# Performance work log

Hardware: AMD Instinct MI355X
Metric: run time of the kernel (lower is better)

The kernel has to match this reference:

```python
import jax, jax.numpy as jnp
import numpy as np
import math

B, N, E, H = 2, 10000, 160000, 128
ET = 8
EPS = 1e-5


def setup_inputs() -> dict:
    key = jax.random.key(0)
    ks = jax.random.split(key, 20)
    s = 1.0 / math.sqrt(H)
    inp = {
        "hidden": jax.random.normal(ks[0], (B, N, H), jnp.float32),
        "time_emb": jax.random.normal(ks[1], (B, N, H), jnp.float32),
        "edge_index": jax.random.randint(ks[2], (2, E), 0, N),
        "edge_type": jax.random.randint(ks[3], (E,), 0, ET),
        # parameters
        "edge_emb": jax.random.normal(ks[4], (ET, H), jnp.float32),
        "Wq": jax.random.normal(ks[5], (H, H), jnp.float32) * s,
        "bq": jnp.zeros((H,), jnp.float32),
        "Wk": jax.random.normal(ks[6], (H, H), jnp.float32) * s,
        "bk": jnp.zeros((H,), jnp.float32),
        "Wv": jax.random.normal(ks[7], (H, H), jnp.float32) * s,
        "bv": jnp.zeros((H,), jnp.float32),
        "We": jax.random.normal(ks[8], (H, 1), jnp.float32) * s,
        "be": jnp.zeros((1,), jnp.float32),
        "W1": jax.random.normal(ks[9], (3 * H, H), jnp.float32) * (1.0 / math.sqrt(3 * H)),
        "b1": jnp.zeros((H,), jnp.float32),
        "W2": jax.random.normal(ks[10], (H, H), jnp.float32) * s,
        "b2": jnp.zeros((H,), jnp.float32),
        "gamma": jnp.ones((H,), jnp.float32),
        "beta": jnp.zeros((H,), jnp.float32),
    }
    return inp


def _forward(hidden, time_emb, edge_index, edge_type, edge_emb,
             Wq, bq, Wk, bk, Wv, bv, We, be, W1, b1, W2, b2, gamma, beta):
    src, tgt = edge_index[0], edge_index[1]
    # edge-wise gathers: [B, E, H]
    src_h = hidden[:, src]
    tgt_h = hidden[:, tgt]
    src_t = time_emb[:, src]
    tgt_t = time_emb[:, tgt]
    edge_h = edge_emb[edge_type][None, :, :]  # [1, E, H] broadcasts over batch

    query = (tgt_h + tgt_t) @ Wq + bq
    key = (src_h + src_t + edge_h) @ Wk + bk
    value = (src_h + edge_h) @ Wv + bv

    logits = jnp.einsum("beh,beh->be", query, key) / math.sqrt(H)
    logits = logits + (edge_h @ We + be)[..., 0]  # edge bias broadcast over batch

    # segment softmax per target node (equivalent to the per-node masked softmax loop)
    lT = logits.T  # [E, B]
    seg_max = jax.ops.segment_max(lT, tgt, num_segments=N)          # [N, B]
    seg_max = jnp.where(jnp.isfinite(seg_max), seg_max, 0.0)
    ex = jnp.exp(lT - seg_max[tgt])                                  # [E, B]
    seg_sum = jax.ops.segment_sum(ex, tgt, num_segments=N)           # [N, B]
    weights = (ex / seg_sum[tgt]).T                                  # [B, E]

    messages = value * weights[..., None]                            # [B, E, H]
    # scatter-add to target nodes
    agg = jax.ops.segment_sum(jnp.swapaxes(messages, 0, 1), tgt, num_segments=N)  # [N, B, H]
    aggregated = jnp.swapaxes(agg, 0, 1)                             # [B, N, H]

    cat = jnp.concatenate([hidden, aggregated, time_emb], axis=-1)   # [B, N, 3H]
    updated = jax.nn.silu(cat @ W1 + b1) @ W2 + b2

    x = hidden + updated  # dropout p=0 -> identity
    mu = jnp.mean(x, axis=-1, keepdims=True)
    var = jnp.var(x, axis=-1, keepdims=True)
    return (x - mu) * jax.lax.rsqrt(var + EPS) * gamma + beta


def reference(hidden, time_emb, edge_index, edge_type, edge_emb,
              Wq, bq, Wk, bk, Wv, bv, We, be, W1, b1, W2, b2, gamma, beta):
    return _forward(hidden, time_emb, edge_index, edge_type, edge_emb,
                    Wq, bq, Wk, bk, Wv, bv, We, be, W1, b1, W2, b2, gamma, beta)
```

## Files before the change

kernel.cpp:

```cpp
#include <hip/hip_runtime.h>
#include <math.h>

constexpr int B_  = 2;
constexpr int N_  = 10000;
constexpr int E_  = 160000;
constexpr int H_  = 128;
constexpr int ET_ = 8;
constexpr float EPS_ = 1e-5f;
constexpr float RSQH = 0.08838834764831845f;

typedef __bf16 bf16x8 __attribute__((ext_vector_type(8)));
typedef short  short8 __attribute__((ext_vector_type(8)));
typedef float  f32x4  __attribute__((ext_vector_type(4)));
typedef unsigned short u16;

__device__ inline u16 bf16b(float f) {
    return __builtin_bit_cast(u16, (__bf16)f);
}

__device__ inline bf16x8 ldfrag(const u16* __restrict__ W, int kc, int nt, int lane) {
    short8 s = *(const short8*)(W + ((kc * 8 + nt) * 64 + lane) * 8);
    return __builtin_bit_cast(bf16x8, s);
}

__global__ __launch_bounds__(256)
void setup_kernel(const float* __restrict__ W1, const float* __restrict__ W2,
                  const float* __restrict__ Wq, const float* __restrict__ Wk,
                  const float* __restrict__ Wv,
                  u16* __restrict__ W1s, u16* __restrict__ W2s,
                  u16* __restrict__ Wqs, u16* __restrict__ Wks, u16* __restrict__ Wvs,
                  const float* __restrict__ edge_emb,
                  const float* __restrict__ bk, const float* __restrict__ bv,
                  const float* __restrict__ We, const float* __restrict__ be,
                  float* __restrict__ Kt, float* __restrict__ Vt, float* __restrict__ eb,
                  const int* __restrict__ tgt, int* __restrict__ hist)
{
    const int bid = blockIdx.x, tid = threadIdx.x;
    if (bid < 56) {
        int unit = bid >> 1, half = bid & 1;
        const float* src; u16* dst; int kc;
        if (unit < 12)      { src = W1; dst = W1s; kc = unit; }
        else if (unit < 16) { src = W2; dst = W2s; kc = unit - 12; }
        else if (unit < 20) { src = Wq; dst = Wqs; kc = unit - 16; }
        else if (unit < 24) { src = Wk; dst = Wks; kc = unit - 20; }
        else                { src = Wv; dst = Wvs; kc = unit - 24; }
        int nt = half * 4 + (tid >> 6), lane = tid & 63;
        int q = lane >> 4, c = lane & 15;
        int kbase = kc * 32 + q * 8;
        int col = nt * 16 + c;
        u16* out = dst + ((kc * 8 + nt) * 64 + lane) * 8;
#pragma unroll
        for (int j = 0; j < 8; ++j)
            out[j] = bf16b(src[(kbase + j) * H_ + col]);
    } else if (bid < 64) {
        int t = bid - 56;
        const float* ep = edge_emb + t * H_;
        __shared__ float red[2];
        int j = tid;
        if (j < 128) {
            float ak = bk[j], av = bv[j];
            for (int d = 0; d < H_; d += 4) {
                float e0 = ep[d], e1 = ep[d+1], e2 = ep[d+2], e3 = ep[d+3];
                ak += e0*Wk[(d+0)*H_+j] + e1*Wk[(d+1)*H_+j] + e2*Wk[(d+2)*H_+j] + e3*Wk[(d+3)*H_+j];
                av += e0*Wv[(d+0)*H_+j] + e1*Wv[(d+1)*H_+j] + e2*Wv[(d+2)*H_+j] + e3*Wv[(d+3)*H_+j];
            }
            Kt[t*H_ + j] = ak;
            Vt[t*H_ + j] = av;
            float pe = ep[j] * We[j];
#pragma unroll
            for (int off = 32; off; off >>= 1) pe += __shfl_xor(pe, off);
            if ((j & 63) == 0) red[j >> 6] = pe;
        }
        __syncthreads();
        if (j == 0) eb[t] = red[0] + red[1] + be[0];
    } else {
        int e = (bid - 64) * 256 + tid;
        if (e < E_) atomicAdd(&hist[tgt[e]], 1);
    }
}

__global__ __launch_bounds__(1024)
void scan_kernel(const int* __restrict__ hist, int* __restrict__ offs,
                 int* __restrict__ cursor)
{
    __shared__ int winc[16];
    const int tid = threadIdx.x, wave = tid >> 6, lane = tid & 63;
    int v[10];
    const int idx0 = tid * 10;
    int tot = 0;
#pragma unroll
    for (int i = 0; i < 10; ++i) {
        int idx = idx0 + i;
        v[i] = (idx < N_) ? hist[idx] : 0;
        tot += v[i];
    }
    int s = tot;
#pragma unroll
    for (int off = 1; off < 64; off <<= 1) {
        int t = __shfl_up(s, off);
        if (lane >= off) s += t;
    }
    if (lane == 63) winc[wave] = s;
    __syncthreads();
    if (tid < 16) {
        int si = winc[tid];
#pragma unroll
        for (int off = 1; off < 16; off <<= 1) {
            int t = __shfl_up(si, off);
            if (tid >= off) si += t;
        }
        winc[tid] = si;
    }
    __syncthreads();
    int wbase = (wave == 0) ? 0 : winc[wave - 1];
    int run = wbase + (s - tot);
#pragma unroll
    for (int i = 0; i < 10; ++i) {
        int idx = idx0 + i;
        if (idx < N_) { offs[idx] = run; cursor[idx] = run; }
        run += v[i];
    }
    if (tid == 0) offs[N_] = winc[15];
}

__global__ __launch_bounds__(256)
void scatter_qkv_kernel(const int* __restrict__ src, const int* __restrict__ tgt,
                        const int* __restrict__ type, int* __restrict__ cursor,
                        int* __restrict__ sorted,
                        const float* __restrict__ hidden, const float* __restrict__ time_emb,
                        const u16* __restrict__ Wqs, const u16* __restrict__ Wks,
                        const u16* __restrict__ Wvs, const float* __restrict__ bq,
                        u16* __restrict__ Q, u16* __restrict__ K, u16* __restrict__ V)
{
    if (blockIdx.x < 625) {
        int e = blockIdx.x * 256 + threadIdx.x;
        if (e < E_) {
            int t = tgt[e];
            int pos = atomicAdd(&cursor[t], 1);
            sorted[pos] = src[e] | (type[e] << 16);
        }
        return;
    }
    const int wv = threadIdx.x >> 6, lane = threadIdx.x & 63;
    const int tile = (blockIdx.x - 625) * 4 + wv;
    if (tile >= (B_ * N_) / 16) return;
    const int nbase = tile * 16;
    const int m = lane & 15, q = lane >> 4;
    const int koff = q * 8;

    bf16x8 aq[4], av[4];
    const float* hp = hidden   + (nbase + m) * H_ + koff;
    const float* tp = time_emb + (nbase + m) * H_ + koff;
#pragma unroll
    for (int kc = 0; kc < 4; ++kc) {
        float4 h0 = *(const float4*)(hp + kc * 32);
        float4 h1 = *(const float4*)(hp + kc * 32 + 4);
        float4 t0 = *(const float4*)(tp + kc * 32);
        float4 t1 = *(const float4*)(tp + kc * 32 + 4);
        bf16x8 fv, fq;
        fv[0]=(__bf16)h0.x; fv[1]=(__bf16)h0.y; fv[2]=(__bf16)h0.z; fv[3]=(__bf16)h0.w;
        fv[4]=(__bf16)h1.x; fv[5]=(__bf16)h1.y; fv[6]=(__bf16)h1.z; fv[7]=(__bf16)h1.w;
        fq[0]=(__bf16)(h0.x+t0.x); fq[1]=(__bf16)(h0.y+t0.y);
        fq[2]=(__bf16)(h0.z+t0.z); fq[3]=(__bf16)(h0.w+t0.w);
        fq[4]=(__bf16)(h1.x+t1.x); fq[5]=(__bf16)(h1.y+t1.y);
        fq[6]=(__bf16)(h1.z+t1.z); fq[7]=(__bf16)(h1.w+t1.w);
        av[kc] = fv; aq[kc] = fq;
    }

    f32x4 accq[8], acck[8], accv[8];
#pragma unroll
    for (int nt = 0; nt < 8; ++nt) { accq[nt] = (f32x4)0.f; acck[nt] = (f32x4)0.f; accv[nt] = (f32x4)0.f; }

#pragma unroll
    for (int kc = 0; kc < 4; ++kc) {
#pragma unroll
        for (int nt = 0; nt < 8; ++nt) {
            bf16x8 bfq = ldfrag(Wqs, kc, nt, lane);
            bf16x8 bfk = ldfrag(Wks, kc, nt, lane);
            bf16x8 bfv = ldfrag(Wvs, kc, nt, lane);
            accq[nt] = __builtin_amdgcn_mfma_f32_16x16x32_bf16(aq[kc], bfq, accq[nt], 0, 0, 0);
            acck[nt] = __builtin_amdgcn_mfma_f32_16x16x32_bf16(aq[kc], bfk, acck[nt], 0, 0, 0);
            accv[nt] = __builtin_amdgcn_mfma_f32_16x16x32_bf16(av[kc], bfv, accv[nt], 0, 0, 0);
        }
    }

#pragma unroll
    for (int nt = 0; nt < 8; ++nt) {
        int col = nt * 16 + m;
        float bqc = bq[col];
#pragma unroll
        for (int r = 0; r < 4; ++r) {
            int node = nbase + q * 4 + r;
            Q[node * H_ + col] = bf16b(accq[nt][r] + bqc);
            K[node * H_ + col] = bf16b(acck[nt][r]);
            V[node * H_ + col] = bf16b(accv[nt][r]);
        }
    }
}

__global__ __launch_bounds__(256)
void attn_kernel(const u16* __restrict__ Qb, const u16* __restrict__ Kb,
                 const u16* __restrict__ Vb,
                 const float* __restrict__ Kt, const float* __restrict__ Vt,
                 const float* __restrict__ eb,
                 const int* __restrict__ offs, const int* __restrict__ sorted,
                 u16* __restrict__ aggb)
{
    __shared__ float bias_s[4][8];
    __shared__ __align__(16) u16 vt_s[8][128];

    const int tid = threadIdx.x;
    const int wv = tid >> 6, lane = tid & 63;
    const int g = lane >> 4, lam = lane & 15;

    for (int idx = tid; idx < ET_ * H_; idx += 256)
        vt_s[idx >> 7][idx & 127] = bf16b(Vt[idx]);
    __syncthreads();

    const int b = blockIdx.x & 1;
    const int n = (blockIdx.x >> 1) * 4 + wv;
    const int bn = b * N_ + n;
    const int beg = offs[n], end = offs[n + 1];
    const u16* __restrict__ Kbb = Kb + (size_t)(b * N_) * H_;
    const u16* __restrict__ Vbb = Vb + (size_t)(b * N_) * H_;

    float q[8];
    {
        short8 s8 = *(const short8*)(Qb + (size_t)bn * H_ + lam * 8);
        bf16x8 qa = __builtin_bit_cast(bf16x8, s8);
#pragma unroll
        for (int j = 0; j < 8; ++j) q[j] = (float)qa[j];
    }

    {
        const float* k0p = Kt + (2 * g) * H_ + lam * 8;
        const float* k1p = Kt + (2 * g + 1) * H_ + lam * 8;
        float p0 = 0.f, p1 = 0.f;
#pragma unroll
        for (int j = 0; j < 8; ++j) { p0 += q[j] * k0p[j]; p1 += q[j] * k1p[j]; }
#pragma unroll
        for (int msk = 1; msk < 16; msk <<= 1) {
            p0 += __shfl_xor(p0, msk);
            p1 += __shfl_xor(p1, msk);
        }
        if (lam == 0) {
            bias_s[wv][2 * g]     = p0 * RSQH + eb[2 * g];
            bias_s[wv][2 * g + 1] = p1 * RSQH + eb[2 * g + 1];
        }
    }

    float m_g = -INFINITY, l_g = 0.f;
    float acc[8];
#pragma unroll
    for (int j = 0; j < 8; ++j) acc[j] = 0.f;

    int c = beg + g;
    for (; c + 4 < end; c += 8) {
        int pk0 = sorted[c];
        int pk1 = sorted[c + 4];
        int s0 = pk0 & 0xFFFF, t0 = pk0 >> 16;
        int s1 = pk1 & 0xFFFF, t1 = pk1 >> 16;
        short8 k80 = *(const short8*)(Kbb + (size_t)s0 * H_ + lam * 8);
        short8 k81 = *(const short8*)(Kbb + (size_t)s1 * H_ + lam * 8);
        short8 v80 = *(const short8*)(Vbb + (size_t)s0 * H_ + lam * 8);
        short8 v81 = *(const short8*)(Vbb + (size_t)s1 * H_ + lam * 8);
        short8 vt80 = *(const short8*)(&vt_s[t0][lam * 8]);
        short8 vt81 = *(const short8*)(&vt_s[t1][lam * 8]);
        bf16x8 ka0 = __builtin_bit_cast(bf16x8, k80);
        bf16x8 ka1 = __builtin_bit_cast(bf16x8, k81);
        float p0 = 0.f, p1 = 0.f;
#pragma unroll
        for (int j = 0; j < 8; ++j) {
            p0 += q[j] * (float)ka0[j];
            p1 += q[j] * (float)ka1[j];
        }
#pragma unroll
        for (int msk = 1; msk < 16; msk <<= 1) {
            p0 += __shfl_xor(p0, msk);
            p1 += __shfl_xor(p1, msk);
        }
        float lg0 = p0 * RSQH + bias_s[wv][t0];
        float lg1 = p1 * RSQH + bias_s[wv][t1];
        float mx = fmaxf(lg0, lg1);
        if (mx > m_g + 8.f) {
            float rs = __expf(m_g - mx);
            l_g *= rs;
#pragma unroll
            for (int j = 0; j < 8; ++j) acc[j] *= rs;
            m_g = mx;
        }
        float w0 = __expf(lg0 - m_g);
        float w1 = __expf(lg1 - m_g);
        l_g += w0 + w1;
        bf16x8 va0  = __builtin_bit_cast(bf16x8, v80);
        bf16x8 va1  = __builtin_bit_cast(bf16x8, v81);
        bf16x8 vta0 = __builtin_bit_cast(bf16x8, vt80);
        bf16x8 vta1 = __builtin_bit_cast(bf16x8, vt81);
#pragma unroll
        for (int j = 0; j < 8; ++j)
            acc[j] += w0 * ((float)va0[j] + (float)vta0[j])
                    + w1 * ((float)va1[j] + (float)vta1[j]);
    }
    if (c < end) {
        int pk0 = sorted[c];
        int s0 = pk0 & 0xFFFF, t0 = pk0 >> 16;
        short8 k80 = *(const short8*)(Kbb + (size_t)s0 * H_ + lam * 8);
        short8 v80 = *(const short8*)(Vbb + (size_t)s0 * H_ + lam * 8);
        short8 vt80 = *(const short8*)(&vt_s[t0][lam * 8]);
        bf16x8 ka0 = __builtin_bit_cast(bf16x8, k80);
        float p0 = 0.f;
#pragma unroll
        for (int j = 0; j < 8; ++j) p0 += q[j] * (float)ka0[j];
#pragma unroll
        for (int msk = 1; msk < 16; msk <<= 1) p0 += __shfl_xor(p0, msk);
        float lg0 = p0 * RSQH + bias_s[wv][t0];
        if (lg0 > m_g + 8.f) {
            float rs = __expf(m_g - lg0);
            l_g *= rs;
#pragma unroll
            for (int j = 0; j < 8; ++j) acc[j] *= rs;
            m_g = lg0;
        }
        float w0 = __expf(lg0 - m_g);
        l_g += w0;
        bf16x8 va0  = __builtin_bit_cast(bf16x8, v80);
        bf16x8 vta0 = __builtin_bit_cast(bf16x8, vt80);
#pragma unroll
        for (int j = 0; j < 8; ++j)
            acc[j] += w0 * ((float)va0[j] + (float)vta0[j]);
    }

    float M = fmaxf(m_g, __shfl_xor(m_g, 16));
    M = fmaxf(M, __shfl_xor(M, 32));
    float rs = (m_g == M) ? 1.f : __expf(m_g - M);
    l_g *= rs;
#pragma unroll
    for (int j = 0; j < 8; ++j) {
        acc[j] *= rs;
        acc[j] += __shfl_xor(acc[j], 16);
        acc[j] += __shfl_xor(acc[j], 32);
    }
    l_g += __shfl_xor(l_g, 16);
    l_g += __shfl_xor(l_g, 32);

    if (g == 0) {
        float invL = (end > beg) ? 1.f / l_g : 0.f;
        bf16x8 o;
#pragma unroll
        for (int j = 0; j < 8; ++j) o[j] = (__bf16)(acc[j] * invL);
        *(short8*)(aggb + (size_t)bn * H_ + lam * 8) = __builtin_bit_cast(short8, o);
    }
}

__global__ __launch_bounds__(256)
void mlp_mfma_kernel(const float* __restrict__ hidden, const u16* __restrict__ aggb,
                     const float* __restrict__ time_emb,
                     const u16* __restrict__ W1s, const u16* __restrict__ W2s,
                     const float* __restrict__ b1, const float* __restrict__ b2,
                     const float* __restrict__ gamma, const float* __restrict__ beta,
                     float* __restrict__ out)
{
    __shared__ __align__(16) u16 h1s[4][16][136];
    const int wv = threadIdx.x >> 6, lane = threadIdx.x & 63;
    const int tile = blockIdx.x * 4 + wv;
    if (tile >= (B_ * N_) / 16) return;
    const int nbase = tile * 16;
    const int m = lane & 15, q = lane >> 4;
    const int koff = q * 8;

    bf16x8 a[12];
    const float* hp = hidden   + (nbase + m) * H_ + koff;
    const float* tp = time_emb + (nbase + m) * H_ + koff;
    const u16*   ap = aggb + (size_t)(nbase + m) * H_ + koff;
#pragma unroll
    for (int kc = 0; kc < 4; ++kc) {
        float4 h0 = *(const float4*)(hp + kc * 32);
        float4 h1 = *(const float4*)(hp + kc * 32 + 4);
        float4 t0 = *(const float4*)(tp + kc * 32);
        float4 t1 = *(const float4*)(tp + kc * 32 + 4);
        bf16x8 fh, ft;
        fh[0]=(__bf16)h0.x; fh[1]=(__bf16)h0.y; fh[2]=(__bf16)h0.z; fh[3]=(__bf16)h0.w;
        fh[4]=(__bf16)h1.x; fh[5]=(__bf16)h1.y; fh[6]=(__bf16)h1.z; fh[7]=(__bf16)h1.w;
        ft[0]=(__bf16)t0.x; ft[1]=(__bf16)t0.y; ft[2]=(__bf16)t0.z; ft[3]=(__bf16)t0.w;
        ft[4]=(__bf16)t1.x; ft[5]=(__bf16)t1.y; ft[6]=(__bf16)t1.z; ft[7]=(__bf16)t1.w;
        a[0 * 4 + kc] = fh;
        a[2 * 4 + kc] = ft;
        short8 s8 = *(const short8*)(ap + kc * 32);
        a[1 * 4 + kc] = __builtin_bit_cast(bf16x8, s8);
    }

    f32x4 acc[8];
#pragma unroll
    for (int nt = 0; nt < 8; ++nt) acc[nt] = (f32x4)0.f;
#pragma unroll
    for (int kc = 0; kc < 12; ++kc) {
#pragma unroll
        for (int nt = 0; nt < 8; ++nt) {
            bf16x8 bf = ldfrag(W1s, kc, nt, lane);
            acc[nt] = __builtin_amdgcn_mfma_f32_16x16x32_bf16(a[kc], bf, acc[nt], 0, 0, 0);
        }
    }

#pragma unroll
    for (int nt = 0; nt < 8; ++nt) {
        int col = nt * 16 + m;
        float bb = b1[col];
#pragma unroll
        for (int r = 0; r < 4; ++r) {
            float v = acc[nt][r] + bb;
            float h = v / (1.f + __expf(-v));
            h1s[wv][q * 4 + r][col] = bf16b(h);
        }
    }

    f32x4 acc2[8];
#pragma unroll
    for (int nt = 0; nt < 8; ++nt) acc2[nt] = (f32x4)0.f;
#pragma unroll
    for (int kc = 0; kc < 4; ++kc) {
        short8 s8 = *(const short8*)&h1s[wv][m][kc * 32 + koff];
        bf16x8 a2 = __builtin_bit_cast(bf16x8, s8);
#pragma unroll
        for (int nt = 0; nt < 8; ++nt) {
            bf16x8 bf = ldfrag(W2s, kc, nt, lane);
            acc2[nt] = __builtin_amdgcn_mfma_f32_16x16x32_bf16(a2, bf, acc2[nt], 0, 0, 0);
        }
    }

    float x[8][4];
#pragma unroll
    for (int nt = 0; nt < 8; ++nt) {
        int col = nt * 16 + m;
        float bb = b2[col];
#pragma unroll
        for (int r = 0; r < 4; ++r) {
            int node = nbase + q * 4 + r;
            x[nt][r] = hidden[node * H_ + col] + acc2[nt][r] + bb;
        }
    }
#pragma unroll
    for (int r = 0; r < 4; ++r) {
        float s = 0.f, ss = 0.f;
#pragma unroll
        for (int nt = 0; nt < 8; ++nt) { s += x[nt][r]; ss += x[nt][r] * x[nt][r]; }
#pragma unroll
        for (int off = 1; off < 16; off <<= 1) {
            s  += __shfl_xor(s, off);
            ss += __shfl_xor(ss, off);
        }
        float mu  = s * (1.f / H_);
        float var = ss * (1.f / H_) - mu * mu;
        float rs  = rsqrtf(var + EPS_);
        int node = nbase + q * 4 + r;
#pragma unroll
        for (int nt = 0; nt < 8; ++nt) {
            int col = nt * 16 + m;
            out[node * H_ + col] = (x[nt][r] - mu) * rs * gamma[col] + beta[col];
        }
    }
}

extern "C" void kernel_launch(void* const* d_in, const int* in_sizes, int n_in,
                              void* d_out, int out_size, void* d_ws, size_t ws_size,
                              hipStream_t stream)
{
    const float* hidden   = (const float*)d_in[0];
    const float* time_emb = (const float*)d_in[1];
    const int*   eidx     = (const int*)d_in[2];
    const int*   etype    = (const int*)d_in[3];
    const float* edge_emb = (const float*)d_in[4];
    const float* Wq = (const float*)d_in[5];
    const float* bq = (const float*)d_in[6];
    const float* Wk = (const float*)d_in[7];
    const float* bk = (const float*)d_in[8];
    const float* Wv = (const float*)d_in[9];
    const float* bv = (const float*)d_in[10];
    const float* We = (const float*)d_in[11];
    const float* be = (const float*)d_in[12];
    const float* W1 = (const float*)d_in[13];
    const float* b1 = (const float*)d_in[14];
    const float* W2 = (const float*)d_in[15];
    const float* b2 = (const float*)d_in[16];
    const float* gamma = (const float*)d_in[17];
    const float* beta  = (const float*)d_in[18];
    float* out = (float*)d_out;

    constexpr int BNH = B_ * N_ * H_;
    u16* Qb   = (u16*)d_ws;
    u16* Kb   = Qb + BNH;
    u16* Vb   = Kb + BNH;
    u16* aggb = Vb + BNH;
    float* Kt  = (float*)(aggb + BNH);
    float* Vt  = Kt + ET_ * H_;
    float* ebt = Vt + ET_ * H_;
    int* hist   = (int*)(ebt + ET_);
    int* offs   = hist + N_;
    int* cursor = offs + (N_ + 1);
    int* sorted = cursor + N_;
    uintptr_t wp = (uintptr_t)(sorted + E_);
    wp = (wp + 15) & ~(uintptr_t)15;
    u16* W1s = (u16*)wp;
    u16* W2s = W1s + 384 * 128;
    u16* Wqs = W2s + 128 * 128;
    u16* Wks = Wqs + 128 * 128;
    u16* Wvs = Wks + 128 * 128;

    const int* esrc = eidx;
    const int* etgt = eidx + E_;

    hipMemsetAsync(hist, 0, N_ * sizeof(int), stream);

    setup_kernel<<<64 + (E_ + 255) / 256, 256, 0, stream>>>(
        W1, W2, Wq, Wk, Wv, W1s, W2s, Wqs, Wks, Wvs,
        edge_emb, bk, bv, We, be, Kt, Vt, ebt, etgt, hist);
    scan_kernel<<<1, 1024, 0, stream>>>(hist, offs, cursor);
    scatter_qkv_kernel<<<625 + 313, 256, 0, stream>>>(
        esrc, etgt, etype, cursor, sorted,
        hidden, time_emb, Wqs, Wks, Wvs, bq, Qb, Kb, Vb);
    attn_kernel<<<(B_ * N_) / 4, 256, 0, stream>>>(Qb, Kb, Vb, Kt, Vt, ebt, offs, sorted, aggb);
    mlp_mfma_kernel<<<313, 256, 0, stream>>>(hidden, aggb, time_emb, W1s, W2s, b1, b2, gamma, beta, out);
}
```

Baseline: 193.1 us.

## Fuse attention aggregation with MLP and LayerNorm into one kernel

Merges the attention kernel and the MLP kernel so that each 256-thread block aggregates 16 nodes (4 per wave) into shared memory and then runs the MLP on that tile. The four waves split the output columns, and the LayerNorm statistics are reduced across waves through shared memory. This removes the bf16 aggregate round trip through global memory and one kernel launch. In exchange, each wave now processes its 4 nodes serially, adds block barriers, and uses fewer blocks (1250 instead of 5000) for the latency-bound gather phase, which may lower latency hiding.

```diff
diff --git a/kernel.cpp b/kernel.cpp
--- a/kernel.cpp
+++ b/kernel.cpp
@@ -199,179 +199,178 @@
 }
 
 __global__ __launch_bounds__(256)
-void attn_kernel(const u16* __restrict__ Qb, const u16* __restrict__ Kb,
-                 const u16* __restrict__ Vb,
-                 const float* __restrict__ Kt, const float* __restrict__ Vt,
-                 const float* __restrict__ eb,
-                 const int* __restrict__ offs, const int* __restrict__ sorted,
-                 u16* __restrict__ aggb)
-{
-    __shared__ float bias_s[4][8];
-    __shared__ __align__(16) u16 vt_s[8][128];
-
-    const int tid = threadIdx.x;
-    const int wv = tid >> 6, lane = tid & 63;
-    const int g = lane >> 4, lam = lane & 15;
-
-    for (int idx = tid; idx < ET_ * H_; idx += 256)
-        vt_s[idx >> 7][idx & 127] = bf16b(Vt[idx]);
-    __syncthreads();
-
-    const int b = blockIdx.x & 1;
-    const int n = (blockIdx.x >> 1) * 4 + wv;
-    const int bn = b * N_ + n;
-    const int beg = offs[n], end = offs[n + 1];
-    const u16* __restrict__ Kbb = Kb + (size_t)(b * N_) * H_;
-    const u16* __restrict__ Vbb = Vb + (size_t)(b * N_) * H_;
-
-    float q[8];
-    {
-        short8 s8 = *(const short8*)(Qb + (size_t)bn * H_ + lam * 8);
-        bf16x8 qa = __builtin_bit_cast(bf16x8, s8);
-#pragma unroll
-        for (int j = 0; j < 8; ++j) q[j] = (float)qa[j];
-    }
-
-    {
-        const float* k0p = Kt + (2 * g) * H_ + lam * 8;
-        const float* k1p = Kt + (2 * g + 1) * H_ + lam * 8;
-        float p0 = 0.f, p1 = 0.f;
-#pragma unroll
-        for (int j = 0; j < 8; ++j) { p0 += q[j] * k0p[j]; p1 += q[j] * k1p[j]; }
-#pragma unroll
-        for (int msk = 1; msk < 16; msk <<= 1) {
-            p0 += __shfl_xor(p0, msk);
-            p1 += __shfl_xor(p1, msk);
-        }
-        if (lam == 0) {
-            bias_s[wv][2 * g]     = p0 * RSQH + eb[2 * g];
-            bias_s[wv][2 * g + 1] = p1 * RSQH + eb[2 * g + 1];
-        }
-    }
-
-    float m_g = -INFINITY, l_g = 0.f;
-    float acc[8];
-#pragma unroll
-    for (int j = 0; j < 8; ++j) acc[j] = 0.f;
-
-    int c = beg + g;
-    for (; c + 4 < end; c += 8) {
-        int pk0 = sorted[c];
-        int pk1 = sorted[c + 4];
-        int s0 = pk0 & 0xFFFF, t0 = pk0 >> 16;
-        int s1 = pk1 & 0xFFFF, t1 = pk1 >> 16;
-        short8 k80 = *(const short8*)(Kbb + (size_t)s0 * H_ + lam * 8);
-        short8 k81 = *(const short8*)(Kbb + (size_t)s1 * H_ + lam * 8);
-        short8 v80 = *(const short8*)(Vbb + (size_t)s0 * H_ + lam * 8);
-        short8 v81 = *(const short8*)(Vbb + (size_t)s1 * H_ + lam * 8);
-        short8 vt80 = *(const short8*)(&vt_s[t0][lam * 8]);
-        short8 vt81 = *(const short8*)(&vt_s[t1][lam * 8]);
-        bf16x8 ka0 = __builtin_bit_cast(bf16x8, k80);
-        bf16x8 ka1 = __builtin_bit_cast(bf16x8, k81);
-        float p0 = 0.f, p1 = 0.f;
-#pragma unroll
-        for (int j = 0; j < 8; ++j) {
-            p0 += q[j] * (float)ka0[j];
-            p1 += q[j] * (float)ka1[j];
-        }
-#pragma unroll
-        for (int msk = 1; msk < 16; msk <<= 1) {
-            p0 += __shfl_xor(p0, msk);
-            p1 += __shfl_xor(p1, msk);
-        }
-        float lg0 = p0 * RSQH + bias_s[wv][t0];
-        float lg1 = p1 * RSQH + bias_s[wv][t1];
-        float mx = fmaxf(lg0, lg1);
-        if (mx > m_g + 8.f) {
-            float rs = __expf(m_g - mx);
-            l_g *= rs;
-#pragma unroll
-            for (int j = 0; j < 8; ++j) acc[j] *= rs;
-            m_g = mx;
-        }
-        float w0 = __expf(lg0 - m_g);
-        float w1 = __expf(lg1 - m_g);
-        l_g += w0 + w1;
-        bf16x8 va0  = __builtin_bit_cast(bf16x8, v80);
-        bf16x8 va1  = __builtin_bit_cast(bf16x8, v81);
-        bf16x8 vta0 = __builtin_bit_cast(bf16x8, vt80);
-        bf16x8 vta1 = __builtin_bit_cast(bf16x8, vt81);
-#pragma unroll
-        for (int j = 0; j < 8; ++j)
-            acc[j] += w0 * ((float)va0[j] + (float)vta0[j])
-                    + w1 * ((float)va1[j] + (float)vta1[j]);
-    }
-    if (c < end) {
-        int pk0 = sorted[c];
-        int s0 = pk0 & 0xFFFF, t0 = pk0 >> 16;
-        short8 k80 = *(const short8*)(Kbb + (size_t)s0 * H_ + lam * 8);
-        short8 v80 = *(const short8*)(Vbb + (size_t)s0 * H_ + lam * 8);
-        short8 vt80 = *(const short8*)(&vt_s[t0][lam * 8]);
-        bf16x8 ka0 = __builtin_bit_cast(bf16x8, k80);
-        float p0 = 0.f;
-#pragma unroll
-        for (int j = 0; j < 8; ++j) p0 += q[j] * (float)ka0[j];
-#pragma unroll
-        for (int msk = 1; msk < 16; msk <<= 1) p0 += __shfl_xor(p0, msk);
-        float lg0 = p0 * RSQH + bias_s[wv][t0];
-        if (lg0 > m_g + 8.f) {
-            float rs = __expf(m_g - lg0);
-            l_g *= rs;
-#pragma unroll
-            for (int j = 0; j < 8; ++j) acc[j] *= rs;
-            m_g = lg0;
-        }
-        float w0 = __expf(lg0 - m_g);
-        l_g += w0;
-        bf16x8 va0  = __builtin_bit_cast(bf16x8, v80);
-        bf16x8 vta0 = __builtin_bit_cast(bf16x8, vt80);
-#pragma unroll
-        for (int j = 0; j < 8; ++j)
-            acc[j] += w0 * ((float)va0[j] + (float)vta0[j]);
-    }
-
-    float M = fmaxf(m_g, __shfl_xor(m_g, 16));
-    M = fmaxf(M, __shfl_xor(M, 32));
-    float rs = (m_g == M) ? 1.f : __expf(m_g - M);
-    l_g *= rs;
-#pragma unroll
-    for (int j = 0; j < 8; ++j) {
-        acc[j] *= rs;
-        acc[j] += __shfl_xor(acc[j], 16);
-        acc[j] += __shfl_xor(acc[j], 32);
-    }
-    l_g += __shfl_xor(l_g, 16);
-    l_g += __shfl_xor(l_g, 32);
-
-    if (g == 0) {
-        float invL = (end > beg) ? 1.f / l_g : 0.f;
-        bf16x8 o;
-#pragma unroll
-        for (int j = 0; j < 8; ++j) o[j] = (__bf16)(acc[j] * invL);
-        *(short8*)(aggb + (size_t)bn * H_ + lam * 8) = __builtin_bit_cast(short8, o);
-    }
-}
-
-__global__ __launch_bounds__(256)
-void mlp_mfma_kernel(const float* __restrict__ hidden, const u16* __restrict__ aggb,
-                     const float* __restrict__ time_emb,
+void attn_mlp_kernel(const u16* __restrict__ Qb, const u16* __restrict__ Kb,
+                     const u16* __restrict__ Vb,
+                     const float* __restrict__ Kt, const float* __restrict__ Vt,
+                     const float* __restrict__ eb,
+                     const int* __restrict__ offs, const int* __restrict__ sorted,
+                     const float* __restrict__ hidden, const float* __restrict__ time_emb,
                      const u16* __restrict__ W1s, const u16* __restrict__ W2s,
                      const float* __restrict__ b1, const float* __restrict__ b2,
                      const float* __restrict__ gamma, const float* __restrict__ beta,
                      float* __restrict__ out)
 {
-    __shared__ __align__(16) u16 h1s[4][16][136];
-    const int wv = threadIdx.x >> 6, lane = threadIdx.x & 63;
-    const int tile = blockIdx.x * 4 + wv;
-    if (tile >= (B_ * N_) / 16) return;
-    const int nbase = tile * 16;
+    __shared__ float bias_s[4][8];
+    __shared__ __align__(16) u16 vt_s[8][128];
+    __shared__ __align__(16) u16 agg_s[16][136];
+    __shared__ __align__(16) u16 h1s[16][136];
+    __shared__ float sp[16][4], ssp[16][4];
+
+    const int tid = threadIdx.x;
+    const int wv = tid >> 6, lane = tid & 63;
+    const int g = lane >> 4, lam = lane & 15;
+
+    for (int idx = tid; idx < ET_ * H_; idx += 256)
+        vt_s[idx >> 7][idx & 127] = bf16b(Vt[idx]);
+    __syncthreads();
+
+    const int nbase = blockIdx.x * 16;
+    const int b = (nbase >= N_) ? 1 : 0;
+    const int n0 = nbase - b * N_;
+    const u16* __restrict__ Kbb = Kb + (size_t)(b * N_) * H_;
+    const u16* __restrict__ Vbb = Vb + (size_t)(b * N_) * H_;
+
+    for (int i = 0; i < 4; ++i) {
+        const int nl = wv * 4 + i;
+        const int n = n0 + nl;
+        const int bn = nbase + nl;
+        const int beg = offs[n], end = offs[n + 1];
+
+        float q[8];
+        {
+            short8 s8 = *(const short8*)(Qb + (size_t)bn * H_ + lam * 8);
+            bf16x8 qa = __builtin_bit_cast(bf16x8, s8);
+#pragma unroll
+            for (int j = 0; j < 8; ++j) q[j] = (float)qa[j];
+        }
+
+        {
+            const float* k0p = Kt + (2 * g) * H_ + lam * 8;
+            const float* k1p = Kt + (2 * g + 1) * H_ + lam * 8;
+            float p0 = 0.f, p1 = 0.f;
+#pragma unroll
+            for (int j = 0; j < 8; ++j) { p0 += q[j] * k0p[j]; p1 += q[j] * k1p[j]; }
+#pragma unroll
+            for (int msk = 1; msk < 16; msk <<= 1) {
+                p0 += __shfl_xor(p0, msk);
+                p1 += __shfl_xor(p1, msk);
+            }
+            if (lam == 0) {
+                bias_s[wv][2 * g]     = p0 * RSQH + eb[2 * g];
+                bias_s[wv][2 * g + 1] = p1 * RSQH + eb[2 * g + 1];
+            }
+        }
+
+        float m_g = -INFINITY, l_g = 0.f;
+        float acc[8];
+#pragma unroll
+        for (int j = 0; j < 8; ++j) acc[j] = 0.f;
+
+        int c = beg + g;
+        for (; c + 4 < end; c += 8) {
+            int pk0 = sorted[c];
+            int pk1 = sorted[c + 4];
+            int s0 = pk0 & 0xFFFF, t0 = pk0 >> 16;
+            int s1 = pk1 & 0xFFFF, t1 = pk1 >> 16;
+            short8 k80 = *(const short8*)(Kbb + (size_t)s0 * H_ + lam * 8);
+            short8 k81 = *(const short8*)(Kbb + (size_t)s1 * H_ + lam * 8);
+            short8 v80 = *(const short8*)(Vbb + (size_t)s0 * H_ + lam * 8);
+            short8 v81 = *(const short8*)(Vbb + (size_t)s1 * H_ + lam * 8);
+            short8 vt80 = *(const short8*)(&vt_s[t0][lam * 8]);
+            short8 vt81 = *(const short8*)(&vt_s[t1][lam * 8]);
+            bf16x8 ka0 = __builtin_bit_cast(bf16x8, k80);
+            bf16x8 ka1 = __builtin_bit_cast(bf16x8, k81);
+            float p0 = 0.f, p1 = 0.f;
+#pragma unroll
+            for (int j = 0; j < 8; ++j) {
+                p0 += q[j] * (float)ka0[j];
+                p1 += q[j] * (float)ka1[j];
+            }
+#pragma unroll
+            for (int msk = 1; msk < 16; msk <<= 1) {
+                p0 += __shfl_xor(p0, msk);
+                p1 += __shfl_xor(p1, msk);
+            }
+            float lg0 = p0 * RSQH + bias_s[wv][t0];
+            float lg1 = p1 * RSQH + bias_s[wv][t1];
+            float mx = fmaxf(lg0, lg1);
+            if (mx > m_g + 8.f) {
+                float rs = __expf(m_g - mx);
+                l_g *= rs;
+#pragma unroll
+                for (int j = 0; j < 8; ++j) acc[j] *= rs;
+                m_g = mx;
+            }
+            float w0 = __expf(lg0 - m_g);
+            float w1 = __expf(lg1 - m_g);
+            l_g += w0 + w1;
+            bf16x8 va0  = __builtin_bit_cast(bf16x8, v80);
+            bf16x8 va1  = __builtin_bit_cast(bf16x8, v81);
+            bf16x8 vta0 = __builtin_bit_cast(bf16x8, vt80);
+            bf16x8 vta1 = __builtin_bit_cast(bf16x8, vt81);
+#pragma unroll
+            for (int j = 0; j < 8; ++j)
+                acc[j] += w0 * ((float)va0[j] + (float)vta0[j])
+                        + w1 * ((float)va1[j] + (float)vta1[j]);
+        }
+        if (c < end) {
+            int pk0 = sorted[c];
+            int s0 = pk0 & 0xFFFF, t0 = pk0 >> 16;
+            short8 k80 = *(const short8*)(Kbb + (size_t)s0 * H_ + lam * 8);
+            short8 v80 = *(const short8*)(Vbb + (size_t)s0 * H_ + lam * 8);
+            short8 vt80 = *(const short8*)(&vt_s[t0][lam * 8]);
+            bf16x8 ka0 = __builtin_bit_cast(bf16x8, k80);
+            float p0 = 0.f;
+#pragma unroll
+            for (int j = 0; j < 8; ++j) p0 += q[j] * (float)ka0[j];
+#pragma unroll
+            for (int msk = 1; msk < 16; msk <<= 1) p0 += __shfl_xor(p0, msk);
+            float lg0 = p0 * RSQH + bias_s[wv][t0];
+            if (lg0 > m_g + 8.f) {
+                float rs = __expf(m_g - lg0);
+                l_g *= rs;
+#pragma unroll
+                for (int j = 0; j < 8; ++j) acc[j] *= rs;
+                m_g = lg0;
+            }
+            float w0 = __expf(lg0 - m_g);
+            l_g += w0;
+            bf16x8 va0  = __builtin_bit_cast(bf16x8, v80);
+            bf16x8 vta0 = __builtin_bit_cast(bf16x8, vt80);
+#pragma unroll
+            for (int j = 0; j < 8; ++j)
+                acc[j] += w0 * ((float)va0[j] + (float)vta0[j]);
+        }
+
+        float M = fmaxf(m_g, __shfl_xor(m_g, 16));
+        M = fmaxf(M, __shfl_xor(M, 32));
+        float rs = (m_g == M) ? 1.f : __expf(m_g - M);
+        l_g *= rs;
+#pragma unroll
+        for (int j = 0; j < 8; ++j) {
+            acc[j] *= rs;
+            acc[j] += __shfl_xor(acc[j], 16);
+            acc[j] += __shfl_xor(acc[j], 32);
+        }
+        l_g += __shfl_xor(l_g, 16);
+        l_g += __shfl_xor(l_g, 32);
+
+        if (g == 0) {
+            float invL = (end > beg) ? 1.f / l_g : 0.f;
+            bf16x8 o;
+#pragma unroll
+            for (int j = 0; j < 8; ++j) o[j] = (__bf16)(acc[j] * invL);
+            *(short8*)(&agg_s[nl][lam * 8]) = __builtin_bit_cast(short8, o);
+        }
+    }
+    __syncthreads();
+
     const int m = lane & 15, q = lane >> 4;
     const int koff = q * 8;
 
     bf16x8 a[12];
-    const float* hp = hidden   + (nbase + m) * H_ + koff;
-    const float* tp = time_emb + (nbase + m) * H_ + koff;
-    const u16*   ap = aggb + (size_t)(nbase + m) * H_ + koff;
+    const float* hp = hidden   + (size_t)(nbase + m) * H_ + koff;
+    const float* tp = time_emb + (size_t)(nbase + m) * H_ + koff;
 #pragma unroll
     for (int kc = 0; kc < 4; ++kc) {
         float4 h0 = *(const float4*)(hp + kc * 32);
@@ -385,77 +384,82 @@
         ft[4]=(__bf16)t1.x; ft[5]=(__bf16)t1.y; ft[6]=(__bf16)t1.z; ft[7]=(__bf16)t1.w;
         a[0 * 4 + kc] = fh;
         a[2 * 4 + kc] = ft;
-        short8 s8 = *(const short8*)(ap + kc * 32);
+        short8 s8 = *(const short8*)(&agg_s[m][kc * 32 + koff]);
         a[1 * 4 + kc] = __builtin_bit_cast(bf16x8, s8);
     }
 
-    f32x4 acc[8];
-#pragma unroll
-    for (int nt = 0; nt < 8; ++nt) acc[nt] = (f32x4)0.f;
+    f32x4 acc1[2];
+    acc1[0] = (f32x4)0.f; acc1[1] = (f32x4)0.f;
 #pragma unroll
     for (int kc = 0; kc < 12; ++kc) {
 #pragma unroll
-        for (int nt = 0; nt < 8; ++nt) {
-            bf16x8 bf = ldfrag(W1s, kc, nt, lane);
-            acc[nt] = __builtin_amdgcn_mfma_f32_16x16x32_bf16(a[kc], bf, acc[nt], 0, 0, 0);
-        }
-    }
-
-#pragma unroll
-    for (int nt = 0; nt < 8; ++nt) {
-        int col = nt * 16 + m;
+        for (int ntl = 0; ntl < 2; ++ntl) {
+            bf16x8 bf = ldfrag(W1s, kc, 2 * wv + ntl, lane);
+            acc1[ntl] = __builtin_amdgcn_mfma_f32_16x16x32_bf16(a[kc], bf, acc1[ntl], 0, 0, 0);
+        }
+    }
+#pragma unroll
+    for (int ntl = 0; ntl < 2; ++ntl) {
+        int col = (2 * wv + ntl) * 16 + m;
         float bb = b1[col];
 #pragma unroll
         for (int r = 0; r < 4; ++r) {
-            float v = acc[nt][r] + bb;
+            float v = acc1[ntl][r] + bb;
             float h = v / (1.f + __expf(-v));
-            h1s[wv][q * 4 + r][col] = bf16b(h);
-        }
-    }
-
-    f32x4 acc2[8];
-#pragma unroll
-    for (int nt = 0; nt < 8; ++nt) acc2[nt] = (f32x4)0.f;
+            h1s[q * 4 + r][col] = bf16b(h);
+        }
+    }
+    __syncthreads();
+
+    f32x4 acc2[2];
+    acc2[0] = (f32x4)0.f; acc2[1] = (f32x4)0.f;
 #pragma unroll
     for (int kc = 0; kc < 4; ++kc) {
-        short8 s8 = *(const short8*)&h1s[wv][m][kc * 32 + koff];
+        short8 s8 = *(const short8*)(&h1s[m][kc * 32 + koff]);
         bf16x8 a2 = __builtin_bit_cast(bf16x8, s8);
 #pragma unroll
-        for (int nt = 0; nt < 8; ++nt) {
-            bf16x8 bf = ldfrag(W2s, kc, nt, lane);
-            acc2[nt] = __builtin_amdgcn_mfma_f32_16x16x32_bf16(a2, bf, acc2[nt], 0, 0, 0);
-        }
-    }
-
-    float x[8][4];
-#pragma unroll
-    for (int nt = 0; nt < 8; ++nt) {
-        int col = nt * 16 + m;
+        for (int ntl = 0; ntl < 2; ++ntl) {
+            bf16x8 bf = ldfrag(W2s, kc, 2 * wv + ntl, lane);
+            acc2[ntl] = __builtin_amdgcn_mfma_f32_16x16x32_bf16(a2, bf, acc2[ntl], 0, 0, 0);
+        }
+    }
+
+    float x[2][4];
+#pragma unroll
+    for (int ntl = 0; ntl < 2; ++ntl) {
+        int col = (2 * wv + ntl) * 16 + m;
         float bb = b2[col];
 #pragma unroll
         for (int r = 0; r < 4; ++r) {
             int node = nbase + q * 4 + r;
-            x[nt][r] = hidden[node * H_ + col] + acc2[nt][r] + bb;
+            x[ntl][r] = hidden[(size_t)node * H_ + col] + acc2[ntl][r] + bb;
         }
     }
 #pragma unroll
     for (int r = 0; r < 4; ++r) {
-        float s = 0.f, ss = 0.f;
-#pragma unroll
-        for (int nt = 0; nt < 8; ++nt) { s += x[nt][r]; ss += x[nt][r] * x[nt][r]; }
+        float s  = x[0][r] + x[1][r];
+        float ss = x[0][r] * x[0][r] + x[1][r] * x[1][r];
 #pragma unroll
         for (int off = 1; off < 16; off <<= 1) {
             s  += __shfl_xor(s, off);
             ss += __shfl_xor(ss, off);
         }
+        if (m == 0) { sp[q * 4 + r][wv] = s; ssp[q * 4 + r][wv] = ss; }
+    }
+    __syncthreads();
+#pragma unroll
+    for (int r = 0; r < 4; ++r) {
+        int nl = q * 4 + r;
+        float s  = sp[nl][0]  + sp[nl][1]  + sp[nl][2]  + sp[nl][3];
+        float ss = ssp[nl][0] + ssp[nl][1] + ssp[nl][2] + ssp[nl][3];
         float mu  = s * (1.f / H_);
         float var = ss * (1.f / H_) - mu * mu;
-        float rs  = rsqrtf(var + EPS_);
-        int node = nbase + q * 4 + r;
-#pragma unroll
-        for (int nt = 0; nt < 8; ++nt) {
-            int col = nt * 16 + m;
-            out[node * H_ + col] = (x[nt][r] - mu) * rs * gamma[col] + beta[col];
+        float rsn = rsqrtf(var + EPS_);
+        int node = nbase + nl;
+#pragma unroll
+        for (int ntl = 0; ntl < 2; ++ntl) {
+            int col = (2 * wv + ntl) * 16 + m;
+            out[(size_t)node * H_ + col] = (x[ntl][r] - mu) * rsn * gamma[col] + beta[col];
         }
     }
 }
@@ -489,8 +493,7 @@
     u16* Qb   = (u16*)d_ws;
     u16* Kb   = Qb + BNH;
     u16* Vb   = Kb + BNH;
-    u16* aggb = Vb + BNH;
-    float* Kt  = (float*)(aggb + BNH);
+    float* Kt  = (float*)(Vb + BNH);
     float* Vt  = Kt + ET_ * H_;
     float* ebt = Vt + ET_ * H_;
     int* hist   = (int*)(ebt + ET_);
@@ -517,6 +520,7 @@
     scatter_qkv_kernel<<<625 + 313, 256, 0, stream>>>(
         esrc, etgt, etype, cursor, sorted,
         hidden, time_emb, Wqs, Wks, Wvs, bq, Qb, Kb, Vb);
-    attn_kernel<<<(B_ * N_) / 4, 256, 0, stream>>>(Qb, Kb, Vb, Kt, Vt, ebt, offs, sorted, aggb);
-    mlp_mfma_kernel<<<313, 256, 0, stream>>>(hidden, aggb, time_emb, W1s, W2s, b1, b2, gamma, beta, out);
-}
+    attn_mlp_kernel<<<(B_ * N_) / 16, 256, 0, stream>>>(
+        Qb, Kb, Vb, Kt, Vt, ebt, offs, sorted,
+        hidden, time_emb, W1s, W2s, b1, b2, gamma, beta, out);
+}
```

Measured after the change: 205.7 us. 1.07x slower.
